# Optimization experiments

Measured on AMD Instinct MI355X. Metric: run time of the kernel, lower is better.

Reference implementation:

```python
import jax, jax.numpy as jnp
import numpy as np

M, K, N = 4096, 4096, 4096

def setup_inputs() -> dict:
    key = jax.random.key(0)
    k1, k2, k3 = jax.random.split(key, 3)
    a = jax.random.randint(k1, (M, K), 0, 127, dtype=jnp.int32)
    b = jax.random.randint(k2, (K, N), 0, 127, dtype=jnp.int32)
    scale = jax.random.uniform(k3, (N,), dtype=jnp.float32)
    return {"a": a, "b": b, "scale": scale}

def reference(a, b, scale):
    a8 = a.astype(jnp.int8)
    b8 = b.astype(jnp.int8)
    acc = jnp.matmul(a8, b8, preferred_element_type=jnp.int32)  # [M, N] int32
    # fused per-column (per-output-channel) dequantization scale
    return acc.astype(jnp.float32) * scale[None, :]  # [M, N] float32
```

## Files before the change

### kernel.cpp

```cpp
#include <hip/hip_runtime.h>
#include <stdint.h>

#define M_DIM 4096
#define K_DIM 4096
#define N_DIM 4096

typedef int v4i __attribute__((ext_vector_type(4)));
typedef int int32x4 __attribute__((ext_vector_type(4)));

__device__ __forceinline__ void gload_lds16(const void* g, void* l) {
    __builtin_amdgcn_global_load_lds(
        (const __attribute__((address_space(1))) uint32_t*)g,
        (__attribute__((address_space(3))) uint32_t*)l, 16, 0, 0);
}

__global__ void pack_ab_kernel(const int* __restrict__ a, char* __restrict__ a8,
                               const int* __restrict__ b, char* __restrict__ b8t) {
    __shared__ char tile[64][68];
    if (blockIdx.x < 2048) {
        int idx = blockIdx.x * 256 + threadIdx.x;
        const int stride = 2048 * 256;
        const int total4 = M_DIM * K_DIM / 4;
        for (int i = idx; i < total4; i += stride) {
            int32x4 v = ((const int32x4*)a)[i];
            uint32_t p = (uint32_t)(v.x & 0xff) | ((uint32_t)(v.y & 0xff) << 8) |
                         ((uint32_t)(v.z & 0xff) << 16) | ((uint32_t)(v.w & 0xff) << 24);
            ((uint32_t*)a8)[i] = p;
        }
    } else {
        int bid2 = blockIdx.x - 2048;
        int n0 = (bid2 & 63) * 64;
        int k0 = (bid2 >> 6) * 64;
        int tx = threadIdx.x & 63;
        int ty = threadIdx.x >> 6;
#pragma unroll
        for (int kk = 0; kk < 64; kk += 4) {
            tile[kk + ty][tx] = (char)b[(size_t)(k0 + kk + ty) * N_DIM + n0 + tx];
        }
        __syncthreads();
        int td = threadIdx.x & 15;
        int tn = threadIdx.x >> 4;
#pragma unroll
        for (int nn0 = 0; nn0 < 64; nn0 += 16) {
            int nn = nn0 + tn;
            uint32_t p = (uint32_t)(uint8_t)tile[td * 4 + 0][nn] |
                         ((uint32_t)(uint8_t)tile[td * 4 + 1][nn] << 8) |
                         ((uint32_t)(uint8_t)tile[td * 4 + 2][nn] << 16) |
                         ((uint32_t)(uint8_t)tile[td * 4 + 3][nn] << 24);
            *(uint32_t*)&b8t[(size_t)(n0 + nn) * K_DIM + k0 + td * 4] = p;
        }
    }
}

#define BM 256
#define BN 256
#define BK 128
#define KTILES (K_DIM / BK)

#define BAR __builtin_amdgcn_s_barrier()
#define WAIT_VM4 asm volatile("s_waitcnt vmcnt(4)" ::: "memory")
#define WAIT_VM2 asm volatile("s_waitcnt vmcnt(2)" ::: "memory")
#define WAIT_VM0 asm volatile("s_waitcnt vmcnt(0)" ::: "memory")

#define DS_A(dst, kk, ib)                                                               \
    _Pragma("unroll") for (int i_ = 0; i_ < 4; ++i_) dst[i_] =                          \
        *(const v4i*)(lds + bufOff + (kk) * 16384 + aOff + ((ib) + i_) * 1024);

#define DS_B(dst, kk)                                                                   \
    _Pragma("unroll") for (int j_ = 0; j_ < 4; ++j_) dst[j_] =                          \
        *(const v4i*)(lds + bufOff + (kk) * 16384 + bOff + j_ * 1024);

#define MM(ib, AF, BF)                                                                  \
    __builtin_amdgcn_s_setprio(1);                                                      \
    _Pragma("unroll") for (int i_ = 0; i_ < 4; ++i_)                                    \
    _Pragma("unroll") for (int j_ = 0; j_ < 4; ++j_)                                    \
        acc[(ib) + i_][j_] =                                                            \
            __builtin_amdgcn_mfma_i32_16x16x64_i8(AF[i_], BF[j_], acc[(ib) + i_][j_],   \
                                                  0, 0, 0);                             \
    __builtin_amdgcn_s_setprio(0);

__global__ __launch_bounds__(512, 2) void gemm_i8_8ph(const char* __restrict__ A8,
                                                      const char* __restrict__ B8T,
                                                      const float* __restrict__ scale,
                                                      float* __restrict__ out) {
    __shared__ char lds[131072];

    int tid = threadIdx.x;
    int wave = tid >> 6;
    int lane = tid & 63;
    int wr = wave >> 2;
    int wc = wave & 3;
    int l15 = lane & 15;

    int bid = blockIdx.x;
    int swz = (bid & 7) * 32 + (bid >> 3);
    int bm = swz >> 4;
    int bn = swz & 15;

    int rA = tid >> 2;
    int cc = ((tid & 3) ^ ((tid >> 3) & 3)) << 4;
    const char* aSrc = A8 + (size_t)(bm * BM + rA) * K_DIM + cc;
    const char* bSrc = B8T + (size_t)(bn * BN + rA) * K_DIM + cc;

    int slot = (((lane >> 4) ^ ((lane >> 1) & 3)) << 4);
    int aOff = wr * 8192 + l15 * 64 + slot;
    int bOff = 32768 + wc * 4096 + l15 * 64 + slot;

    v4i acc[8][4];
#pragma unroll
    for (int i = 0; i < 8; ++i)
#pragma unroll
        for (int j = 0; j < 4; ++j) acc[i][j] = (v4i){0, 0, 0, 0};

    auto stage = [&](const char* srcBase, int kt1, int kk, int dstOff) {
        const char* s = srcBase + (size_t)kt1 * BK + kk * 64;
        char* d = (char*)lds + dstOff + wave * 1024;
        gload_lds16(s, d);
        gload_lds16(s + (size_t)128 * K_DIM, d + 8192);
    };

    stage(aSrc, 0, 0, 0);
    stage(bSrc, 0, 0, 32768);
    stage(aSrc, 0, 1, 16384);
    stage(bSrc, 0, 1, 49152);
    WAIT_VM4;
    BAR;

    int bufOff = 0;
    v4i a03[4], a47[4], b0[4];
    v4i a03n[4], a47n[4], b0n[4];

    for (int kt = 0; kt < KTILES - 1; ++kt) {
        int nbufOff = bufOff ^ 65536;
        DS_A(a03, 0, 0);
        DS_B(b0, 0);
        DS_A(a47, 0, 4);
        stage(aSrc, kt + 1, 0, nbufOff + 0);
        BAR;
        MM(0, a03, b0);
        WAIT_VM2;
        BAR;
        DS_A(a03n, 1, 0);
        DS_B(b0n, 1);
        stage(bSrc, kt + 1, 0, nbufOff + 32768);
        BAR;
        MM(4, a47, b0);
        BAR;
        DS_A(a47n, 1, 4);
        stage(aSrc, kt + 1, 1, nbufOff + 16384);
        BAR;
        MM(0, a03n, b0n);
        BAR;
        stage(bSrc, kt + 1, 1, nbufOff + 49152);
        BAR;
        MM(4, a47n, b0n);
        WAIT_VM4;
        BAR;
        bufOff = nbufOff;
    }

    DS_A(a03, 0, 0);
    DS_B(b0, 0);
    DS_A(a47, 0, 4);
    MM(0, a03, b0);
    MM(4, a47, b0);
    WAIT_VM0;
    BAR;
    DS_A(a03n, 1, 0);
    DS_B(b0n, 1);
    DS_A(a47n, 1, 4);
    MM(0, a03n, b0n);
    MM(4, a47n, b0n);

    size_t orow0 = (size_t)bm * BM + wr * 128 + (lane >> 4) * 4;
    int ocol0 = bn * BN + wc * 64 + l15;
#pragma unroll
    for (int j = 0; j < 4; ++j) {
        int col = ocol0 + j * 16;
        float s = scale[col];
#pragma unroll
        for (int i = 0; i < 8; ++i) {
            size_t row = orow0 + (size_t)i * 16;
#pragma unroll
            for (int r = 0; r < 4; ++r) {
                out[(row + r) * N_DIM + col] = (float)acc[i][j][r] * s;
            }
        }
    }
}

#define FBM 128
#define FBN 128
#define FBK 64

__global__ __launch_bounds__(256) void gemm_i8_fused_kernel(const int* __restrict__ a,
                                                            const int* __restrict__ b,
                                                            const float* __restrict__ scale,
                                                            float* __restrict__ out) {
    __shared__ char As[FBM * FBK];
    __shared__ char Bs[FBN * FBK];

    int tid = threadIdx.x;
    int wave = tid >> 6;
    int lane = tid & 63;

    int nwg = gridDim.x;
    int cpx = nwg >> 3;
    int bid = blockIdx.x;
    int swz = (bid & 7) * cpx + (bid >> 3);
    int bm = swz >> 5;
    int bn = swz & 31;

    int f0 = tid * 16;
    int m0 = f0 >> 6;
    int k0 = f0 & 63;

    int nn = tid & 127;
    int kh = tid >> 7;

    int wr = wave >> 1;
    int wc = wave & 1;
    int lrow = lane & 15;
    int kgrp = (lane >> 4) * 16;

    v4i acc[4][4];
#pragma unroll
    for (int i = 0; i < 4; ++i)
#pragma unroll
        for (int j = 0; j < 4; ++j) acc[i][j] = (v4i){0, 0, 0, 0};

    const int kTiles = K_DIM / FBK;
    for (int kt = 0; kt < kTiles; ++kt) {
        __syncthreads();
#pragma unroll
        for (int r = 0; r < 2; ++r) {
            const int* src = a + (size_t)(bm * FBM + m0 + r * 64) * K_DIM + kt * FBK + k0;
            uint32_t pk[4];
#pragma unroll
            for (int q = 0; q < 4; ++q) {
                int32x4 v = *(const int32x4*)(src + q * 4);
                pk[q] = (uint32_t)(v.x & 0xff) | ((uint32_t)(v.y & 0xff) << 8) |
                        ((uint32_t)(v.z & 0xff) << 16) | ((uint32_t)(v.w & 0xff) << 24);
            }
            *(v4i*)&As[f0 + r * 4096] = (v4i){(int)pk[0], (int)pk[1], (int)pk[2], (int)pk[3]};
        }
#pragma unroll
        for (int d = 0; d < 8; ++d) {
            uint32_t p = 0;
#pragma unroll
            for (int i = 0; i < 4; ++i) {
                int kk = kt * FBK + kh * 32 + d * 4 + i;
                p |= (uint32_t)(b[(size_t)kk * N_DIM + bn * FBN + nn] & 0xff) << (8 * i);
            }
            *(uint32_t*)&Bs[nn * 64 + kh * 32 + d * 4] = p;
        }
        __syncthreads();

        v4i aF[4], bF[4];
#pragma unroll
        for (int i = 0; i < 4; ++i)
            aF[i] = *(const v4i*)&As[(wr * 64 + i * 16 + lrow) * FBK + kgrp];
#pragma unroll
        for (int j = 0; j < 4; ++j)
            bF[j] = *(const v4i*)&Bs[(wc * 64 + j * 16 + lrow) * FBK + kgrp];
#pragma unroll
        for (int i = 0; i < 4; ++i)
#pragma unroll
            for (int j = 0; j < 4; ++j)
                acc[i][j] = __builtin_amdgcn_mfma_i32_16x16x64_i8(aF[i], bF[j], acc[i][j], 0, 0, 0);
    }

    size_t orow0 = (size_t)bm * FBM + wr * 64;
    int ocol0 = bn * FBN + wc * 64;
#pragma unroll
    for (int j = 0; j < 4; ++j) {
        int col = ocol0 + j * 16 + lrow;
        float s = scale[col];
#pragma unroll
        for (int i = 0; i < 4; ++i) {
            size_t row = orow0 + i * 16 + (lane >> 4) * 4;
#pragma unroll
            for (int r = 0; r < 4; ++r) {
                out[(row + r) * N_DIM + col] = (float)acc[i][j][r] * s;
            }
        }
    }
}

extern "C" void kernel_launch(void* const* d_in, const int* in_sizes, int n_in,
                              void* d_out, int out_size, void* d_ws, size_t ws_size,
                              hipStream_t stream) {
    const int* a = (const int*)d_in[0];
    const int* b = (const int*)d_in[1];
    const float* scale = (const float*)d_in[2];
    float* out = (float*)d_out;

    size_t need = (size_t)M_DIM * K_DIM + (size_t)K_DIM * N_DIM;
    if (ws_size >= need) {
        char* a8 = (char*)d_ws;
        char* b8t = a8 + (size_t)M_DIM * K_DIM;
        pack_ab_kernel<<<2048 + 4096, 256, 0, stream>>>(a, a8, b, b8t);
        gemm_i8_8ph<<<256, 512, 0, stream>>>(a8, b8t, scale, out);
    } else {
        gemm_i8_fused_kernel<<<1024, 256, 0, stream>>>(a, b, scale, out);
    }
}
```

Before: 95.94 us.

## Replace eight-phase barrier schedule with two-phase slip schedule per K-tile

```diff
diff --git a/kernel.cpp b/kernel.cpp
--- a/kernel.cpp
+++ b/kernel.cpp
@@ -59,7 +59,6 @@
 
 #define BAR __builtin_amdgcn_s_barrier()
 #define WAIT_VM4 asm volatile("s_waitcnt vmcnt(4)" ::: "memory")
-#define WAIT_VM2 asm volatile("s_waitcnt vmcnt(2)" ::: "memory")
 #define WAIT_VM0 asm volatile("s_waitcnt vmcnt(0)" ::: "memory")
 
 #define DS_A(dst, kk, ib)                                                               \
@@ -79,10 +78,10 @@
                                                   0, 0, 0);                             \
     __builtin_amdgcn_s_setprio(0);
 
-__global__ __launch_bounds__(512, 2) void gemm_i8_8ph(const char* __restrict__ A8,
-                                                      const char* __restrict__ B8T,
-                                                      const float* __restrict__ scale,
-                                                      float* __restrict__ out) {
+__global__ __launch_bounds__(512, 2) void gemm_i8_slip(const char* __restrict__ A8,
+                                                       const char* __restrict__ B8T,
+                                                       const float* __restrict__ scale,
+                                                       float* __restrict__ out) {
     __shared__ char lds[131072];
 
     int tid = threadIdx.x;
@@ -128,32 +127,25 @@
 
     int bufOff = 0;
     v4i a03[4], a47[4], b0[4];
-    v4i a03n[4], a47n[4], b0n[4];
 
     for (int kt = 0; kt < KTILES - 1; ++kt) {
         int nbufOff = bufOff ^ 65536;
+        stage(aSrc, kt + 1, 0, nbufOff + 0);
+        stage(bSrc, kt + 1, 0, nbufOff + 32768);
         DS_A(a03, 0, 0);
         DS_B(b0, 0);
         DS_A(a47, 0, 4);
-        stage(aSrc, kt + 1, 0, nbufOff + 0);
+        MM(0, a03, b0);
+        MM(4, a47, b0);
+        WAIT_VM4;
         BAR;
+        stage(aSrc, kt + 1, 1, nbufOff + 16384);
+        stage(bSrc, kt + 1, 1, nbufOff + 49152);
+        DS_A(a03, 1, 0);
+        DS_B(b0, 1);
+        DS_A(a47, 1, 4);
         MM(0, a03, b0);
-        WAIT_VM2;
-        BAR;
-        DS_A(a03n, 1, 0);
-        DS_B(b0n, 1);
-        stage(bSrc, kt + 1, 0, nbufOff + 32768);
-        BAR;
         MM(4, a47, b0);
-        BAR;
-        DS_A(a47n, 1, 4);
-        stage(aSrc, kt + 1, 1, nbufOff + 16384);
-        BAR;
-        MM(0, a03n, b0n);
-        BAR;
-        stage(bSrc, kt + 1, 1, nbufOff + 49152);
-        BAR;
-        MM(4, a47n, b0n);
         WAIT_VM4;
         BAR;
         bufOff = nbufOff;
@@ -166,11 +158,11 @@
     MM(4, a47, b0);
     WAIT_VM0;
     BAR;
-    DS_A(a03n, 1, 0);
-    DS_B(b0n, 1);
-    DS_A(a47n, 1, 4);
-    MM(0, a03n, b0n);
-    MM(4, a47n, b0n);
+    DS_A(a03, 1, 0);
+    DS_B(b0, 1);
+    DS_A(a47, 1, 4);
+    MM(0, a03, b0);
+    MM(4, a47, b0);
 
     size_t orow0 = (size_t)bm * BM + wr * 128 + (lane >> 4) * 4;
     int ocol0 = bn * BN + wc * 64 + l15;
@@ -300,7 +292,7 @@
         char* a8 = (char*)d_ws;
         char* b8t = a8 + (size_t)M_DIM * K_DIM;
         pack_ab_kernel<<<2048 + 4096, 256, 0, stream>>>(a, a8, b, b8t);
-        gemm_i8_8ph<<<256, 512, 0, stream>>>(a8, b8t, scale, out);
+        gemm_i8_slip<<<256, 512, 0, stream>>>(a8, b8t, scale, out);
     } else {
         gemm_i8_fused_kernel<<<1024, 256, 0, stream>>>(a, b, scale, out);
     }
```

After: 97.44 us. No clear change (+1.6%).
